# Kernel optimization log

Measured on AMD Instinct MI355X. Metric: run time of the kernel, lower is better.

Reference implementation:

```python
import jax, jax.numpy as jnp
import numpy as np

N, M, D = 100000, 50000, 256
NE = N + M
B = 131072

def kl_normal_std(mu, scale):
    # KL( N(mu, scale) || N(0, 1) ) = -log(scale) + (scale^2 + mu^2)/2 - 1/2
    return 0.5 * (scale * scale + mu * mu - 1.0) - jnp.log(scale)

def setup_inputs() -> dict:
    key = jax.random.key(0)
    ks = jax.random.split(key, 8)
    users = jax.random.randint(ks[0], (B, 1), 0, N)
    items = jax.random.randint(ks[1], (B, 1), N, NE)
    x = jnp.concatenate([users, items], axis=1)                        # [B, 2]
    bias_table = jax.random.normal(ks[2], (NE, 2), dtype=jnp.float32)
    entity_table = jax.random.normal(ks[3], (NE, 2 * D), dtype=jnp.float32)
    global_bias_mean = jnp.zeros((1,), dtype=jnp.float32)
    global_bias_scale = jnp.ones((1,), dtype=jnp.float32)
    nb_occ = jax.random.randint(ks[4], (NE,), 1, 1001)                 # train occurrence counts >= 1
    eps_bias = jax.random.normal(ks[5], (NE,), dtype=jnp.float32)
    eps_entity = jax.random.normal(ks[6], (NE, D), dtype=jnp.float32)
    eps_global = jax.random.normal(ks[7], (1,), dtype=jnp.float32)
    return {"x": x, "bias_table": bias_table, "entity_table": entity_table,
            "global_bias_mean": global_bias_mean, "global_bias_scale": global_bias_scale,
            "nb_occ": nb_occ, "eps_bias": eps_bias, "eps_entity": eps_entity,
            "eps_global": eps_global}

def reference(x, bias_table, entity_table, global_bias_mean, global_bias_scale,
              nb_occ, eps_bias, eps_entity, eps_global):
    # --- reparameterized samples (one eps per table row == one eps per unique entity) ---
    gb_scale = jnp.abs(global_bias_scale)
    global_bias = global_bias_mean + gb_scale * eps_global             # [1]

    bias_mu = bias_table[:, 0]
    bias_sc = jnp.abs(bias_table[:, 1])
    biases_all = bias_mu + bias_sc * eps_bias                          # [NE]

    ent_mu = entity_table[:, :D]
    ent_sc = jnp.abs(entity_table[:, D:])
    entities_all = ent_mu + ent_sc * eps_entity                        # [NE, D]

    # --- FM forward: bias sum + product-sum interaction ---
    pair_bias = biases_all[x].sum(axis=1)                              # [B]
    pair_emb = (entities_all[x[:, 0]] * entities_all[x[:, 1]]).sum(axis=1)  # [B]
    logits = global_bias + pair_bias + pair_emb                        # [B] (Bernoulli logits)

    # --- closed-form KL vs N(0,1), rescaled by batch/train occupancy ---
    kl_bias = kl_normal_std(bias_mu, bias_sc)                          # [NE]
    kl_entity = kl_normal_std(ent_mu, ent_sc).sum(axis=1)              # [NE]

    nb_occ_f = nb_occ.astype(jnp.float32)
    cnt = jnp.bincount(x.reshape(-1), length=NE).astype(jnp.float32)   # nb_occ_in_batch
    cnt_u = jnp.bincount(x[:, 0], length=NE).astype(jnp.float32)
    cnt_i = jnp.bincount(x[:, 1], length=NE).astype(jnp.float32)
    user_norm = (cnt_u / nb_occ_f).sum()
    item_norm = (cnt_i / nb_occ_f).sum()

    ids = jnp.arange(NE)
    scale_term = (jnp.where(ids <= N, float(N), 0.0) / user_norm
                  + jnp.where(ids > N, float(M), 0.0) / item_norm)
    kl_rescaled = ((kl_bias + kl_entity) * (cnt / nb_occ_f) * scale_term).sum()

    kl_global = kl_normal_std(global_bias_mean, gb_scale).sum()
    return logits, kl_global + kl_rescaled
```

## Files before the change

kernel.cpp:

```cpp
#include <hip/hip_runtime.h>
#include <math.h>

#define NU   100000
#define MI   50000
#define NEn  150000
#define Bp   131072

typedef float    f4v __attribute__((ext_vector_type(4)));
typedef _Float16 h8v __attribute__((ext_vector_type(8)));
typedef _Float16 h4v __attribute__((ext_vector_type(4)));

__device__ __forceinline__ float wred(float v) {
#pragma unroll
    for (int m = 32; m > 0; m >>= 1) v += __shfl_xor(v, m, 64);
    return v;
}
__device__ __forceinline__ float hred(float v) {
#pragma unroll
    for (int m = 16; m > 0; m >>= 1) v += __shfl_xor(v, m, 64);
    return v;
}

__global__ __launch_bounds__(256) void k_count(const int* __restrict__ x,
                                               int* __restrict__ cnt,
                                               const float* __restrict__ gbm,
                                               const float* __restrict__ gbs,
                                               float* __restrict__ outkl) {
    int t = blockIdx.x * 256 + threadIdx.x;
    if (t < 2 * Bp) atomicAdd(cnt + x[t], 1);
    if (t == 0) {
        float gm = gbm[0];
        float gs = fabsf(gbs[0]);
        outkl[0] = 0.5f * (gs * gs + gm * gm - 1.0f) - __logf(gs);
    }
}

__global__ __launch_bounds__(256) void k_entnorm(
    const f4v* __restrict__ et,
    const f4v* __restrict__ epse,
    const float* __restrict__ bt,
    const float* __restrict__ epsb,
    const int*   __restrict__ cnt,
    const int*   __restrict__ nb,
    h4v*   __restrict__ enth,
    float* __restrict__ biases,
    float* __restrict__ klpe,
    float* __restrict__ hdr)
{
    if (blockIdx.x >= NEn / 4) {
        int e = (blockIdx.x - NEn / 4) * 256 + threadIdx.x;
        float uv = 0.f, iv = 0.f;
        if (e < NEn) {
            float v = (float)cnt[e] / (float)nb[e];
            if (e < NU) uv = v; else iv = v;
        }
        uv = wred(uv);
        iv = wred(iv);
        if ((threadIdx.x & 63) == 0) {
            if (uv != 0.f) atomicAdd(hdr + 0, uv);
            if (iv != 0.f) atomicAdd(hdr + 1, iv);
        }
        return;
    }

    int lane = threadIdx.x & 63;
    int e    = blockIdx.x * 4 + (threadIdx.x >> 6);
    if (cnt[e] == 0) return;

    const f4v* row = et + (size_t)e * 128;
    f4v mu = __builtin_nontemporal_load(row + lane);
    f4v s4 = __builtin_nontemporal_load(row + 64 + lane);
    f4v ep = __builtin_nontemporal_load(epse + (size_t)e * 64 + lane);
    float scx = fabsf(s4.x), scy = fabsf(s4.y), scz = fabsf(s4.z), scw = fabsf(s4.w);

    if (enth) {
        float ox = fmaf(scx, ep.x, mu.x);
        float oy = fmaf(scy, ep.y, mu.y);
        float oz = fmaf(scz, ep.z, mu.z);
        float ow = fmaf(scw, ep.w, mu.w);
        h4v oh;
        oh.x = (_Float16)ox; oh.y = (_Float16)oy;
        oh.z = (_Float16)oz; oh.w = (_Float16)ow;
        enth[(size_t)e * 64 + lane] = oh;
    }

    float kl = 0.5f * (scx * scx + mu.x * mu.x - 1.0f) - __logf(scx)
             + 0.5f * (scy * scy + mu.y * mu.y - 1.0f) - __logf(scy)
             + 0.5f * (scz * scz + mu.z * mu.z - 1.0f) - __logf(scz)
             + 0.5f * (scw * scw + mu.w * mu.w - 1.0f) - __logf(scw);
    kl = wred(kl);

    if (lane == 0) {
        float bmu = bt[2 * e];
        float bsc = fabsf(bt[2 * e + 1]);
        biases[e] = fmaf(bsc, epsb[e], bmu);
        klpe[e]   = kl + 0.5f * (bsc * bsc + bmu * bmu - 1.0f) - __logf(bsc);
    }
}

__global__ __launch_bounds__(256) void k_logred(
    const int* __restrict__ x,
    const h8v* __restrict__ enth,
    const float* __restrict__ biases,
    const float* __restrict__ gbm, const float* __restrict__ gbs,
    const float* __restrict__ epsg,
    const float* __restrict__ klpe, const int* __restrict__ cnt,
    const int* __restrict__ nb, const float* __restrict__ hdr,
    float* __restrict__ out)
{
    if (blockIdx.x >= Bp / 8) {
        int e = (blockIdx.x - Bp / 8) * 256 + threadIdx.x;
        float t = 0.f;
        if (e < NEn) {
            int c = cnt[e];
            if (c != 0) {
                float sc = (e <= NU) ? ((float)NU / hdr[0]) : ((float)MI / hdr[1]);
                t = klpe[e] * ((float)c / (float)nb[e]) * sc;
            }
        }
        t = wred(t);
        if ((threadIdx.x & 63) == 0 && t != 0.f) atomicAdd(out + Bp, t);
        return;
    }

    int lane = threadIdx.x & 63;
    int sub  = lane & 31;
    int p    = blockIdx.x * 8 + ((threadIdx.x >> 6) << 1) + (lane >> 5);
    int u = x[2 * p], v = x[2 * p + 1];
    float bu = biases[u];
    float bv = biases[v];
    h8v a = enth[(size_t)u * 32 + sub];
    h8v b = enth[(size_t)v * 32 + sub];
    float d = 0.f;
#pragma unroll
    for (int i = 0; i < 8; ++i) d = fmaf((float)a[i], (float)b[i], d);
    d = hred(d);
    if (sub == 0) {
        float gb = fmaf(fabsf(gbs[0]), epsg[0], gbm[0]);
        out[p] = gb + bu + bv + d;
    }
}

__global__ __launch_bounds__(256) void k_logits_rc(
    const int* __restrict__ x, const float4* __restrict__ et,
    const float4* __restrict__ epse, const float* __restrict__ biases,
    const float* __restrict__ gbm, const float* __restrict__ gbs,
    const float* __restrict__ epsg, float* __restrict__ out)
{
    int lane = threadIdx.x & 63;
    int p    = blockIdx.x * 4 + (threadIdx.x >> 6);
    int u = x[2 * p], v = x[2 * p + 1];
    const float4* ru = et + (size_t)u * 128;
    const float4* rv = et + (size_t)v * 128;
    float4 mu_u = ru[lane], s_u = ru[64 + lane], e_u = epse[(size_t)u * 64 + lane];
    float4 mu_v = rv[lane], s_v = rv[64 + lane], e_v = epse[(size_t)v * 64 + lane];
    float ax = fmaf(fabsf(s_u.x), e_u.x, mu_u.x), bx = fmaf(fabsf(s_v.x), e_v.x, mu_v.x);
    float ay = fmaf(fabsf(s_u.y), e_u.y, mu_u.y), by = fmaf(fabsf(s_v.y), e_v.y, mu_v.y);
    float az = fmaf(fabsf(s_u.z), e_u.z, mu_u.z), bz = fmaf(fabsf(s_v.z), e_v.z, mu_v.z);
    float aw = fmaf(fabsf(s_u.w), e_u.w, mu_u.w), bw = fmaf(fabsf(s_v.w), e_v.w, mu_v.w);
    float d = ax * bx + ay * by + az * bz + aw * bw;
    d = wred(d);
    if (lane == 0) {
        float gb = fmaf(fabsf(gbs[0]), epsg[0], gbm[0]);
        out[p] = gb + biases[u] + biases[v] + d;
    }
}

__global__ __launch_bounds__(256) void k_klred(
    const float* __restrict__ klpe, const int* __restrict__ cnt,
    const int* __restrict__ nb, const float* __restrict__ hdr,
    float* __restrict__ outkl)
{
    int e = blockIdx.x * 256 + threadIdx.x;
    float t = 0.f;
    if (e < NEn) {
        int c = cnt[e];
        if (c != 0) {
            float sc = (e <= NU) ? ((float)NU / hdr[0]) : ((float)MI / hdr[1]);
            t = klpe[e] * ((float)c / (float)nb[e]) * sc;
        }
    }
    t = wred(t);
    if ((threadIdx.x & 63) == 0 && t != 0.f) atomicAdd(outkl, t);
}

extern "C" void kernel_launch(void* const* d_in, const int* in_sizes, int n_in,
                              void* d_out, int out_size, void* d_ws, size_t ws_size,
                              hipStream_t stream)
{
    const int*   x    = (const int*)d_in[0];
    const float* bt   = (const float*)d_in[1];
    const float* et   = (const float*)d_in[2];
    const float* gbm  = (const float*)d_in[3];
    const float* gbs  = (const float*)d_in[4];
    const int*   nb   = (const int*)d_in[5];
    const float* epsb = (const float*)d_in[6];
    const float* epse = (const float*)d_in[7];
    const float* epsg = (const float*)d_in[8];
    float* out = (float*)d_out;

    char*  ws   = (char*)d_ws;
    float* hdr  = (float*)ws;
    int*   cnt  = (int*)  (ws + 64);
    float* klpe = (float*)(ws + 64 + (size_t)NEn * 4);
    float* bia  = (float*)(ws + 64 + (size_t)NEn * 8);
    size_t entoff = 64 + (size_t)NEn * 12;
    h4v* enth = nullptr;
    if (ws_size >= entoff + (size_t)NEn * 512)
        enth = (h4v*)(ws + entoff);

    const int NORMB = (NEn + 255) / 256;

    (void)hipMemsetAsync(ws, 0, 64 + (size_t)NEn * 4, stream);

    k_count<<<(2 * Bp + 255) / 256, 256, 0, stream>>>(x, cnt, gbm, gbs, out + Bp);

    k_entnorm<<<NEn / 4 + NORMB, 256, 0, stream>>>(
        (const f4v*)et, (const f4v*)epse, bt, epsb, cnt, nb,
        enth, bia, klpe, hdr);

    if (enth) {
        k_logred<<<Bp / 8 + NORMB, 256, 0, stream>>>(
            x, (const h8v*)enth, bia, gbm, gbs, epsg,
            klpe, cnt, nb, hdr, out);
    } else {
        k_logits_rc<<<Bp / 4, 256, 0, stream>>>(x, (const float4*)et,
                                                (const float4*)epse, bia,
                                                gbm, gbs, epsg, out);
        k_klred<<<NORMB, 256, 0, stream>>>(klpe, cnt, nb, hdr, out + Bp);
    }
}
```

Before: 572.7 us.

## Fuse counting into entity kernel and restructure KL reduction with final fixup

Merges the histogram count kernel into the entity sampling/KL kernel by dedicating leading blocks to vectorised atomic counting, and folds the occupancy normalisation sums into the logits kernel, with a tiny final kernel applying the per-half rescaling. Because counting now runs concurrently, entity rows are processed unconditionally, dropping the skip for entities absent from the batch. This trades one launch and a dependency stage for extra reads and writes of unused entity rows. Block-level shared reductions cut atomic traffic.

```diff
diff --git a/kernel.cpp b/kernel.cpp
--- a/kernel.cpp
+++ b/kernel.cpp
@@ -6,6 +6,11 @@
 #define NEn  150000
 #define Bp   131072
 
+#define CB   256
+#define EB   (NEn / 4)
+#define TB   ((NEn + 255) / 256)
+#define LB   (Bp / 8)
+
 typedef float    f4v __attribute__((ext_vector_type(4)));
 typedef _Float16 h8v __attribute__((ext_vector_type(8)));
 typedef _Float16 h4v __attribute__((ext_vector_type(4)));
@@ -21,51 +26,37 @@
     return v;
 }
 
-__global__ __launch_bounds__(256) void k_count(const int* __restrict__ x,
-                                               int* __restrict__ cnt,
-                                               const float* __restrict__ gbm,
-                                               const float* __restrict__ gbs,
-                                               float* __restrict__ outkl) {
-    int t = blockIdx.x * 256 + threadIdx.x;
-    if (t < 2 * Bp) atomicAdd(cnt + x[t], 1);
-    if (t == 0) {
-        float gm = gbm[0];
-        float gs = fabsf(gbs[0]);
-        outkl[0] = 0.5f * (gs * gs + gm * gm - 1.0f) - __logf(gs);
-    }
-}
-
-__global__ __launch_bounds__(256) void k_entnorm(
+__global__ __launch_bounds__(256) void k_cnt_ent(
+    const int4* __restrict__ x4,
     const f4v* __restrict__ et,
     const f4v* __restrict__ epse,
     const float* __restrict__ bt,
     const float* __restrict__ epsb,
-    const int*   __restrict__ cnt,
-    const int*   __restrict__ nb,
+    const float* __restrict__ gbm,
+    const float* __restrict__ gbs,
+    int*   __restrict__ cnt,
     h4v*   __restrict__ enth,
-    float* __restrict__ biases,
+    float* __restrict__ bia,
     float* __restrict__ klpe,
-    float* __restrict__ hdr)
-{
-    if (blockIdx.x >= NEn / 4) {
-        int e = (blockIdx.x - NEn / 4) * 256 + threadIdx.x;
-        float uv = 0.f, iv = 0.f;
-        if (e < NEn) {
-            float v = (float)cnt[e] / (float)nb[e];
-            if (e < NU) uv = v; else iv = v;
-        }
-        uv = wred(uv);
-        iv = wred(iv);
-        if ((threadIdx.x & 63) == 0) {
-            if (uv != 0.f) atomicAdd(hdr + 0, uv);
-            if (iv != 0.f) atomicAdd(hdr + 1, iv);
+    float* __restrict__ outkl)
+{
+    if (blockIdx.x < CB) {
+        int t = blockIdx.x * 256 + threadIdx.x;
+        int4 v = x4[t];
+        atomicAdd(cnt + v.x, 1);
+        atomicAdd(cnt + v.y, 1);
+        atomicAdd(cnt + v.z, 1);
+        atomicAdd(cnt + v.w, 1);
+        if (t == 0) {
+            float gm = gbm[0];
+            float gs = fabsf(gbs[0]);
+            outkl[0] = 0.5f * (gs * gs + gm * gm - 1.0f) - __logf(gs);
         }
         return;
     }
 
     int lane = threadIdx.x & 63;
-    int e    = blockIdx.x * 4 + (threadIdx.x >> 6);
-    if (cnt[e] == 0) return;
+    int e    = (blockIdx.x - CB) * 4 + (threadIdx.x >> 6);
 
     const f4v* row = et + (size_t)e * 128;
     f4v mu = __builtin_nontemporal_load(row + lane);
@@ -74,13 +65,11 @@
     float scx = fabsf(s4.x), scy = fabsf(s4.y), scz = fabsf(s4.z), scw = fabsf(s4.w);
 
     if (enth) {
-        float ox = fmaf(scx, ep.x, mu.x);
-        float oy = fmaf(scy, ep.y, mu.y);
-        float oz = fmaf(scz, ep.z, mu.z);
-        float ow = fmaf(scw, ep.w, mu.w);
         h4v oh;
-        oh.x = (_Float16)ox; oh.y = (_Float16)oy;
-        oh.z = (_Float16)oz; oh.w = (_Float16)ow;
+        oh.x = (_Float16)fmaf(scx, ep.x, mu.x);
+        oh.y = (_Float16)fmaf(scy, ep.y, mu.y);
+        oh.z = (_Float16)fmaf(scz, ep.z, mu.z);
+        oh.w = (_Float16)fmaf(scw, ep.w, mu.w);
         enth[(size_t)e * 64 + lane] = oh;
     }
 
@@ -93,42 +82,52 @@
     if (lane == 0) {
         float bmu = bt[2 * e];
         float bsc = fabsf(bt[2 * e + 1]);
-        biases[e] = fmaf(bsc, epsb[e], bmu);
-        klpe[e]   = kl + 0.5f * (bsc * bsc + bmu * bmu - 1.0f) - __logf(bsc);
-    }
-}
-
-__global__ __launch_bounds__(256) void k_logred(
+        bia[e]  = fmaf(bsc, epsb[e], bmu);
+        klpe[e] = kl + 0.5f * (bsc * bsc + bmu * bmu - 1.0f) - __logf(bsc);
+    }
+}
+
+__global__ __launch_bounds__(256) void k_log_tail(
     const int* __restrict__ x,
     const h8v* __restrict__ enth,
-    const float* __restrict__ biases,
+    const float* __restrict__ bia,
     const float* __restrict__ gbm, const float* __restrict__ gbs,
     const float* __restrict__ epsg,
-    const float* __restrict__ klpe, const int* __restrict__ cnt,
-    const int* __restrict__ nb, const float* __restrict__ hdr,
+    const int* __restrict__ cnt, const int* __restrict__ nb,
+    const float* __restrict__ klpe,
+    float* __restrict__ hdr,
     float* __restrict__ out)
 {
-    if (blockIdx.x >= Bp / 8) {
-        int e = (blockIdx.x - Bp / 8) * 256 + threadIdx.x;
-        float t = 0.f;
+    if (blockIdx.x < TB) {
+        int e = blockIdx.x * 256 + threadIdx.x;
+        float u = 0.f, i = 0.f, aa = 0.f, bb = 0.f;
         if (e < NEn) {
-            int c = cnt[e];
-            if (c != 0) {
-                float sc = (e <= NU) ? ((float)NU / hdr[0]) : ((float)MI / hdr[1]);
-                t = klpe[e] * ((float)c / (float)nb[e]) * sc;
-            }
-        }
-        t = wred(t);
-        if ((threadIdx.x & 63) == 0 && t != 0.f) atomicAdd(out + Bp, t);
+            float v  = (float)cnt[e] / (float)nb[e];
+            float kv = klpe[e] * v;
+            if (e < NU)  u  = v;  else i  = v;
+            if (e <= NU) aa = kv; else bb = kv;
+        }
+        u = wred(u); i = wred(i); aa = wred(aa); bb = wred(bb);
+        __shared__ float s[4][4];
+        int wib = threadIdx.x >> 6;
+        if ((threadIdx.x & 63) == 0) {
+            s[wib][0] = u; s[wib][1] = i; s[wib][2] = aa; s[wib][3] = bb;
+        }
+        __syncthreads();
+        if (threadIdx.x < 4) {
+            float t = s[0][threadIdx.x] + s[1][threadIdx.x]
+                    + s[2][threadIdx.x] + s[3][threadIdx.x];
+            if (t != 0.f) atomicAdd(hdr + threadIdx.x, t);
+        }
         return;
     }
 
     int lane = threadIdx.x & 63;
     int sub  = lane & 31;
-    int p    = blockIdx.x * 8 + ((threadIdx.x >> 6) << 1) + (lane >> 5);
+    int p    = (blockIdx.x - TB) * 8 + ((threadIdx.x >> 6) << 1) + (lane >> 5);
     int u = x[2 * p], v = x[2 * p + 1];
-    float bu = biases[u];
-    float bv = biases[v];
+    float bu = bia[u];
+    float bv = bia[v];
     h8v a = enth[(size_t)u * 32 + sub];
     h8v b = enth[(size_t)v * 32 + sub];
     float d = 0.f;
@@ -137,13 +136,18 @@
     d = hred(d);
     if (sub == 0) {
         float gb = fmaf(fabsf(gbs[0]), epsg[0], gbm[0]);
-        out[p] = gb + bu + bv + d;
-    }
+        __builtin_nontemporal_store(gb + bu + bv + d, out + p);
+    }
+}
+
+__global__ void k_fin(const float* __restrict__ hdr, float* __restrict__ outkl) {
+    if (threadIdx.x == 0)
+        outkl[0] += (float)NU * hdr[2] / hdr[0] + (float)MI * hdr[3] / hdr[1];
 }
 
 __global__ __launch_bounds__(256) void k_logits_rc(
     const int* __restrict__ x, const float4* __restrict__ et,
-    const float4* __restrict__ epse, const float* __restrict__ biases,
+    const float4* __restrict__ epse, const float* __restrict__ bia,
     const float* __restrict__ gbm, const float* __restrict__ gbs,
     const float* __restrict__ epsg, float* __restrict__ out)
 {
@@ -162,26 +166,8 @@
     d = wred(d);
     if (lane == 0) {
         float gb = fmaf(fabsf(gbs[0]), epsg[0], gbm[0]);
-        out[p] = gb + biases[u] + biases[v] + d;
-    }
-}
-
-__global__ __launch_bounds__(256) void k_klred(
-    const float* __restrict__ klpe, const int* __restrict__ cnt,
-    const int* __restrict__ nb, const float* __restrict__ hdr,
-    float* __restrict__ outkl)
-{
-    int e = blockIdx.x * 256 + threadIdx.x;
-    float t = 0.f;
-    if (e < NEn) {
-        int c = cnt[e];
-        if (c != 0) {
-            float sc = (e <= NU) ? ((float)NU / hdr[0]) : ((float)MI / hdr[1]);
-            t = klpe[e] * ((float)c / (float)nb[e]) * sc;
-        }
-    }
-    t = wred(t);
-    if ((threadIdx.x & 63) == 0 && t != 0.f) atomicAdd(outkl, t);
+        out[p] = gb + bia[u] + bia[v] + d;
+    }
 }
 
 extern "C" void kernel_launch(void* const* d_in, const int* in_sizes, int n_in,
@@ -209,24 +195,23 @@
     if (ws_size >= entoff + (size_t)NEn * 512)
         enth = (h4v*)(ws + entoff);
 
-    const int NORMB = (NEn + 255) / 256;
-
     (void)hipMemsetAsync(ws, 0, 64 + (size_t)NEn * 4, stream);
 
-    k_count<<<(2 * Bp + 255) / 256, 256, 0, stream>>>(x, cnt, gbm, gbs, out + Bp);
-
-    k_entnorm<<<NEn / 4 + NORMB, 256, 0, stream>>>(
-        (const f4v*)et, (const f4v*)epse, bt, epsb, cnt, nb,
-        enth, bia, klpe, hdr);
+    k_cnt_ent<<<CB + EB, 256, 0, stream>>>(
+        (const int4*)x, (const f4v*)et, (const f4v*)epse, bt, epsb,
+        gbm, gbs, cnt, enth, bia, klpe, out + Bp);
 
     if (enth) {
-        k_logred<<<Bp / 8 + NORMB, 256, 0, stream>>>(
+        k_log_tail<<<TB + LB, 256, 0, stream>>>(
             x, (const h8v*)enth, bia, gbm, gbs, epsg,
-            klpe, cnt, nb, hdr, out);
+            cnt, nb, klpe, hdr, out);
     } else {
+        k_log_tail<<<TB, 256, 0, stream>>>(
+            x, nullptr, bia, gbm, gbs, epsg, cnt, nb, klpe, hdr, out);
         k_logits_rc<<<Bp / 4, 256, 0, stream>>>(x, (const float4*)et,
                                                 (const float4*)epse, bia,
                                                 gbm, gbs, epsg, out);
-        k_klred<<<NORMB, 256, 0, stream>>>(klpe, cnt, nb, hdr, out + Bp);
-    }
-}
+    }
+
+    k_fin<<<1, 64, 0, stream>>>(hdr, out + Bp);
+}
```

New measurement: 529.5 us. 7.5% less time.
